# Kernel optimization log

Measured on AMD Instinct MI355X. Metric: run time of the kernel, lower is better.

The kernel has to match this reference:

```python
import jax, jax.numpy as jnp
import numpy as np

HEADS = 16
DIM_HEAD = 64
QUERY_DIM = 1024
INNER = HEADS * DIM_HEAD
SCALE = DIM_HEAD ** -0.5


def setup_inputs() -> dict:
    key = jax.random.key(0)
    ks = jax.random.split(key, 6)
    B, N, M = 2, 2048, 2048
    x = jax.random.normal(ks[0], (B, N, QUERY_DIM), dtype=jnp.float32)
    context = jax.random.normal(ks[1], (B, M, QUERY_DIM), dtype=jnp.float32)
    s = QUERY_DIM ** -0.5
    # weights stored [in, out] so y = x @ W matches torch Linear(x) with W = weight.T
    Wq = jax.random.normal(ks[2], (QUERY_DIM, INNER), dtype=jnp.float32) * s
    Wk = jax.random.normal(ks[3], (QUERY_DIM, INNER), dtype=jnp.float32) * s
    Wv = jax.random.normal(ks[4], (QUERY_DIM, INNER), dtype=jnp.float32) * s
    Wo = jax.random.normal(ks[5], (INNER, QUERY_DIM), dtype=jnp.float32) * (INNER ** -0.5)
    return {"x": x, "context": context, "Wq": Wq, "Wk": Wk, "Wv": Wv, "Wo": Wo}


def reference(x, context, Wq, Wk, Wv, Wo):
    B, N, _ = x.shape
    M = context.shape[1]
    # projections -> [b, n, h, d]
    q = (x @ Wq).reshape(B, N, HEADS, DIM_HEAD)
    k = (context @ Wk).reshape(B, M, HEADS, DIM_HEAD)
    v = (context @ Wv).reshape(B, M, HEADS, DIM_HEAD)
    sim = jnp.einsum('bihd,bjhd->bhij', q, k) * SCALE  # [b, h, n, m]
    attn = jax.nn.softmax(sim, axis=-1)
    out = jnp.einsum('bhij,bjhd->bihd', attn, v)  # [b, n, h, d]
    out = out.reshape(B, N, INNER)
    return out @ Wo
```

## Files before the change

kernel.cpp:

```cpp
#include <hip/hip_runtime.h>
#include <hip/hip_bf16.h>


typedef __attribute__((ext_vector_type(8))) __bf16    bf16x8;
typedef __attribute__((ext_vector_type(4))) __bf16    bf16x4;
typedef __attribute__((ext_vector_type(4))) float     f32x4;

#define B_    2
#define H_    16
#define N_    2048
#define M_    2048
#define D_    64
#define QD_   1024

#define QSCALE 0.18033688011112042f

__device__ __forceinline__ void gld16(const __bf16* g, __bf16* l) {
    __builtin_amdgcn_global_load_lds(
        (const __attribute__((address_space(1))) unsigned int*)(g),
        (__attribute__((address_space(3))) unsigned int*)(l), 16, 0, 0);
}

__global__ __launch_bounds__(256) void prep(const float* __restrict__ x,
                                            const float* __restrict__ ctx,
                                            const float* __restrict__ w0,
                                            const float* __restrict__ w1,
                                            const float* __restrict__ w2,
                                            const float* __restrict__ w3,
                                            __bf16* __restrict__ xb,
                                            __bf16* __restrict__ cb,
                                            __bf16* __restrict__ t0,
                                            __bf16* __restrict__ t1,
                                            __bf16* __restrict__ t2,
                                            __bf16* __restrict__ t3) {
    __shared__ float tile[64][65];
    const int z = blockIdx.z;
    if (z < 2) {
        const float* src = z ? ctx : x;
        __bf16*      dst = z ? cb  : xb;
        const size_t base = (size_t)(blockIdx.y * 16 + blockIdx.x) * 16384;
#pragma unroll
        for (int p = 0; p < 16; ++p) {
            size_t i = base + p * 1024 + threadIdx.x * 4;
            float4 v = *reinterpret_cast<const float4*>(src + i);
            bf16x4 o;
            o.x = (__bf16)v.x; o.y = (__bf16)v.y; o.z = (__bf16)v.z; o.w = (__bf16)v.w;
            *reinterpret_cast<bf16x4*>(dst + i) = o;
        }
        return;
    }
    const int w = z - 2;
    const float* in = (w == 0) ? w0 : (w == 1) ? w1 : (w == 2) ? w2 : w3;
    __bf16*     out = (w == 0) ? t0 : (w == 1) ? t1 : (w == 2) ? t2 : t3;
    const int i0 = blockIdx.x * 64;
    const int o0 = blockIdx.y * 64;
    const int t  = threadIdx.x;
    const int r  = t >> 4;
    const int c4 = (t & 15) * 4;
#pragma unroll
    for (int p = 0; p < 4; ++p) {
        int row = p * 16 + r;
        float4 v = *reinterpret_cast<const float4*>(in + (size_t)(i0 + row) * QD_ + o0 + c4);
        tile[row][c4 + 0] = v.x; tile[row][c4 + 1] = v.y;
        tile[row][c4 + 2] = v.z; tile[row][c4 + 3] = v.w;
    }
    __syncthreads();
#pragma unroll
    for (int p = 0; p < 4; ++p) {
        int orow = p * 16 + r;
        bf16x4 o;
        o.x = (__bf16)tile[c4 + 0][orow];
        o.y = (__bf16)tile[c4 + 1][orow];
        o.z = (__bf16)tile[c4 + 2][orow];
        o.w = (__bf16)tile[c4 + 3][orow];
        *reinterpret_cast<bf16x4*>(out + (size_t)(o0 + orow) * QD_ + i0 + c4) = o;
    }
}

#define GEMM_BODY(A_, Bt_)                                                                     \
    __shared__ __align__(16) __bf16 Alds[2][128 * 32];                                         \
    __shared__ __align__(16) __bf16 Blds[2][64 * 32];                                          \
    const int tid  = threadIdx.x;                                                              \
    const int wid  = tid >> 6;                                                                 \
    const int lane = tid & 63;                                                                 \
    const int l15  = lane & 15;                                                                \
    const int lg   = lane >> 4;                                                                \
    const int wr   = wid >> 1;                                                                 \
    const int wc   = wid & 1;                                                                  \
    const int rowBase = blockIdx.x * 128;                                                      \
    const int colBase = blockIdx.y * 64;                                                       \
    const int srowA = wid * 32 + (lane >> 2);                                                  \
    const int srowB = wid * 16 + (lane >> 2);                                                  \
    const int sgA   = ((lane & 3) ^ ((srowA >> 1) & 3)) * 8;                                   \
    const int sgB   = ((lane & 3) ^ ((srowB >> 1) & 3)) * 8;                                   \
    const __bf16* Ag  = A_  + (size_t)(rowBase + srowA) * QD_ + sgA;                           \
    const __bf16* Ag2 = Ag  + (size_t)16 * QD_;        \
    const __bf16* Bg  = Bt_ + (size_t)(colBase + srowB) * QD_ + sgB;                           \
    const int sOffA  = (wid * 32) * 32;                                                        \
    const int sOffA2 = sOffA + 16 * 32;                                                        \
    const int sOffB  = (wid * 16) * 32;                                                        \
    int aoff[4], boff[2];                                                                      \
    _Pragma("unroll")                                                                          \
    for (int m = 0; m < 4; ++m) {                                                              \
        int ra = wr * 64 + m * 16 + l15;                                                       \
        aoff[m] = ra * 32 + ((lg ^ ((ra >> 1) & 3)) * 8);                                      \
    }                                                                                          \
    _Pragma("unroll")                                                                          \
    for (int n = 0; n < 2; ++n) {                                                              \
        int rb = wc * 32 + n * 16 + l15;                                                       \
        boff[n] = rb * 32 + ((lg ^ ((rb >> 1) & 3)) * 8);                                      \
    }                                                                                          \
    f32x4 acc[4][2] = {};                                                                      \
    gld16(Ag,  &Alds[0][sOffA]);                                                               \
    gld16(Ag2, &Alds[0][sOffA2]);                                                              \
    gld16(Bg,  &Blds[0][sOffB]);                                                               \
    __syncthreads();                                                                           \
    for (int t = 0; t < 32; t += 2) {                                                          \
        if (t + 1 < 32) {                                                                      \
            int kn = (t + 1) * 32;                                                             \
            gld16(Ag + kn,  &Alds[1][sOffA]);                                                  \
            gld16(Ag2 + kn, &Alds[1][sOffA2]);                                                 \
            gld16(Bg + kn,  &Blds[1][sOffB]);                                                  \
        }                                                                                      \
        GCOMPUTE(0)                                                                            \
        __syncthreads();                                                                       \
        if (t + 2 < 32) {                                                                      \
            int kn = (t + 2) * 32;                                                             \
            gld16(Ag + kn,  &Alds[0][sOffA]);                                                  \
            gld16(Ag2 + kn, &Alds[0][sOffA2]);                                                 \
            gld16(Bg + kn,  &Blds[0][sOffB]);                                                  \
        }                                                                                      \
        GCOMPUTE(1)                                                                            \
        __syncthreads();                                                                       \
    }

#define GCOMPUTE(BUF)                                                                          \
    {                                                                                          \
        bf16x8 a[4], b[2];                                                                     \
        _Pragma("unroll")                                                                      \
        for (int m = 0; m < 4; ++m)                                                            \
            a[m] = *reinterpret_cast<const bf16x8*>(&Alds[BUF][aoff[m]]);                      \
        _Pragma("unroll")                                                                      \
        for (int n = 0; n < 2; ++n)                                                            \
            b[n] = *reinterpret_cast<const bf16x8*>(&Blds[BUF][boff[n]]);                      \
        _Pragma("unroll")                                                                      \
        for (int m = 0; m < 4; ++m)                                                            \
            _Pragma("unroll")                                                                  \
            for (int n = 0; n < 2; ++n)                                                        \
                acc[m][n] = __builtin_amdgcn_mfma_f32_16x16x32_bf16(a[m], b[n], acc[m][n], 0, 0, 0); \
    }

__global__ __launch_bounds__(256) void gemm_qkv(const __bf16* __restrict__ xb,
                                                const __bf16* __restrict__ cb,
                                                const __bf16* __restrict__ Wtq,
                                                const __bf16* __restrict__ Wtk,
                                                const __bf16* __restrict__ Wtv,
                                                __bf16* __restrict__ Qb,
                                                __bf16* __restrict__ Kb,
                                                __bf16* __restrict__ Vt) {
    const int z = blockIdx.z;
    const __bf16* Asel = (z == 0) ? xb : cb;
    const __bf16* Bsel = (z == 0) ? Wtq : (z == 1) ? Wtk : Wtv;
    GEMM_BODY(Asel, Bsel)
#pragma unroll
    for (int m = 0; m < 4; ++m)
#pragma unroll
        for (int n = 0; n < 2; ++n)
#pragma unroll
            for (int r = 0; r < 4; ++r) {
                int rr = rowBase + wr * 64 + m * 16 + lg * 4 + r;
                int cc = colBase + wc * 32 + n * 16 + l15;
                float v = acc[m][n][r];
                int b_ = rr >> 11, nn = rr & 2047, hh = cc >> 6, dd = cc & 63;
                if (z == 0) {
                    Qb[((size_t)(b_ * H_ + hh) * N_ + nn) * D_ + dd] = (__bf16)(v * QSCALE);
                } else if (z == 1) {
                    Kb[((size_t)(b_ * H_ + hh) * N_ + nn) * D_ + dd] = (__bf16)v;
                } else {
                    Vt[((size_t)(b_ * H_ + hh) * D_ + dd) * M_ + nn] = (__bf16)v;
                }
            }
}

__global__ __launch_bounds__(256) void gemm_out(const __bf16* __restrict__ AO,
                                                const __bf16* __restrict__ Wto,
                                                float* __restrict__ out) {
    GEMM_BODY(AO, Wto)
#pragma unroll
    for (int m = 0; m < 4; ++m)
#pragma unroll
        for (int n = 0; n < 2; ++n)
#pragma unroll
            for (int r = 0; r < 4; ++r) {
                int rr = rowBase + wr * 64 + m * 16 + lg * 4 + r;
                int cc = colBase + wc * 32 + n * 16 + l15;
                out[(size_t)rr * QD_ + cc] = acc[m][n][r];
            }
}

__global__ __launch_bounds__(512, 4) void attn_kernel(const __bf16* __restrict__ Q,
                                                      const __bf16* __restrict__ K,
                                                      const __bf16* __restrict__ Vt,
                                                      __bf16* __restrict__ AO) {
    __shared__ __align__(16) __bf16 Klds[2][4096];
    __shared__ __align__(16) __bf16 Vlds[2][4096];

    const int logical = (blockIdx.x & 7) * 64 + (blockIdx.x >> 3);
    const int qt   = logical & 15;
    const int bh   = logical >> 4;
    const int b    = bh >> 4;
    const int h    = bh & 15;
    const int wid  = threadIdx.x >> 6;
    const int lane = threadIdx.x & 63;
    const int l15  = lane & 15;
    const int lg   = lane >> 4;
    const int qbase = qt * 128 + wid * 16;

    const __bf16* Qp = Q  + ((size_t)bh * N_ + qbase) * D_;
    const __bf16* Kp = K  + (size_t)bh * M_ * D_;
    const __bf16* Vp = Vt + (size_t)bh * D_ * M_;

    const int rg   = lane >> 3;
    const int ch   = lane & 7;
    const int skw  = (rg & 3) | ((wid & 1) << 2);
    const int kc   = (ch ^ skw) << 3;
    const int vc   = (ch ^ rg) << 3;
    const int srow = wid * 8 + rg;
    const int ldst = wid * 512;

#define STAGE(BUF, KV0)                                                        \
    gld16(Kp + (size_t)((KV0) + srow) * D_ + kc, &Klds[BUF][ldst]);            \
    gld16(Vp + (size_t)srow * M_ + (KV0) + vc,  &Vlds[BUF][ldst]);

    const int rm0 = ((l15 >> 2) * 8) + (l15 & 3);
    const int sq  = (l15 & 7) << 3;
    const int ak00 = rm0 * 64 + (( 0 + lg * 8) ^ sq);
    const int ak01 = rm0 * 64 + ((32 + lg * 8) ^ sq);
    const int ak10 = ak00 + 256;
    const int ak11 = ak01 + 256;
    const int av0 = l15 * 64 + (( 0 + lg * 8) ^ sq);
    const int av1 = l15 * 64 + ((32 + lg * 8) ^ sq);

    bf16x8 qf0 = *reinterpret_cast<const bf16x8*>(Qp + (size_t)l15 * D_ +      lg * 8);
    bf16x8 qf1 = *reinterpret_cast<const bf16x8*>(Qp + (size_t)l15 * D_ + 32 + lg * 8);

    bf16x8 onesf;
#pragma unroll
    for (int j = 0; j < 8; ++j) onesf[j] = (__bf16)1.0f;

    f32x4 o0 = {}, o1 = {}, o2 = {}, o3 = {}, ors = {};

#define COMPUTE(KB, VB, KOFF, AV)                                                               \
    {                                                                                           \
        bf16x8 k00 = *reinterpret_cast<const bf16x8*>((KB) + ak00 + (KOFF));                    \
        bf16x8 k01 = *reinterpret_cast<const bf16x8*>((KB) + ak01 + (KOFF));                    \
        bf16x8 k10 = *reinterpret_cast<const bf16x8*>((KB) + ak10 + (KOFF));                    \
        bf16x8 k11 = *reinterpret_cast<const bf16x8*>((KB) + ak11 + (KOFF));                    \
        bf16x8 v0  = *reinterpret_cast<const bf16x8*>((VB) + (AV));                             \
        bf16x8 v1  = *reinterpret_cast<const bf16x8*>((VB) + (AV) + 1024);                      \
        bf16x8 v2  = *reinterpret_cast<const bf16x8*>((VB) + (AV) + 2048);                      \
        bf16x8 v3  = *reinterpret_cast<const bf16x8*>((VB) + (AV) + 3072);                      \
        f32x4 s0 = {}, s1 = {};                                                                 \
        s0 = __builtin_amdgcn_mfma_f32_16x16x32_bf16(k00, qf0, s0, 0, 0, 0);                    \
        s0 = __builtin_amdgcn_mfma_f32_16x16x32_bf16(k01, qf1, s0, 0, 0, 0);                    \
        s1 = __builtin_amdgcn_mfma_f32_16x16x32_bf16(k10, qf0, s1, 0, 0, 0);                    \
        s1 = __builtin_amdgcn_mfma_f32_16x16x32_bf16(k11, qf1, s1, 0, 0, 0);                    \
        bf16x8 pf;                                                                              \
        pf[0] = (__bf16)__builtin_amdgcn_exp2f(s0[0]);                                          \
        pf[1] = (__bf16)__builtin_amdgcn_exp2f(s0[1]);                                          \
        pf[2] = (__bf16)__builtin_amdgcn_exp2f(s0[2]);                                          \
        pf[3] = (__bf16)__builtin_amdgcn_exp2f(s0[3]);                                          \
        pf[4] = (__bf16)__builtin_amdgcn_exp2f(s1[0]);                                          \
        pf[5] = (__bf16)__builtin_amdgcn_exp2f(s1[1]);                                          \
        pf[6] = (__bf16)__builtin_amdgcn_exp2f(s1[2]);                                          \
        pf[7] = (__bf16)__builtin_amdgcn_exp2f(s1[3]);                                          \
        ors = __builtin_amdgcn_mfma_f32_16x16x32_bf16(pf, onesf, ors, 0, 0, 0);                 \
        o0 = __builtin_amdgcn_mfma_f32_16x16x32_bf16(pf, v0, o0, 0, 0, 0);                      \
        o1 = __builtin_amdgcn_mfma_f32_16x16x32_bf16(pf, v1, o1, 0, 0, 0);                      \
        o2 = __builtin_amdgcn_mfma_f32_16x16x32_bf16(pf, v2, o2, 0, 0, 0);                      \
        o3 = __builtin_amdgcn_mfma_f32_16x16x32_bf16(pf, v3, o3, 0, 0, 0);                      \
    }

    STAGE(0, 0)
    __syncthreads();

    for (int t = 0; t < 32; t += 2) {
        if (t + 1 < 32) { STAGE(1, (t + 1) * 64) }
        COMPUTE(Klds[0], Vlds[0], 0,    av0)
        COMPUTE(Klds[0], Vlds[0], 2048, av1)
        __syncthreads();
        if (t + 2 < 32) { STAGE(0, (t + 2) * 64) }
        COMPUTE(Klds[1], Vlds[1], 0,    av0)
        COMPUTE(Klds[1], Vlds[1], 2048, av1)
        __syncthreads();
    }
#undef STAGE
#undef COMPUTE

#pragma unroll
    for (int r = 0; r < 4; ++r) {
        float inv = 1.0f / ors[r];
        size_t row = ((size_t)b * N_ + qbase + lg * 4 + r) * QD_ + h * D_ + l15;
        AO[row +  0] = (__bf16)(o0[r] * inv);
        AO[row + 16] = (__bf16)(o1[r] * inv);
        AO[row + 32] = (__bf16)(o2[r] * inv);
        AO[row + 48] = (__bf16)(o3[r] * inv);
    }
}

extern "C" void kernel_launch(void* const* d_in, const int* in_sizes, int n_in,
                              void* d_out, int out_size, void* d_ws, size_t ws_size,
                              hipStream_t stream) {
    const float* x   = (const float*)d_in[0];
    const float* ctx = (const float*)d_in[1];
    const float* Wq  = (const float*)d_in[2];
    const float* Wk  = (const float*)d_in[3];
    const float* Wv  = (const float*)d_in[4];
    const float* Wo  = (const float*)d_in[5];

    char* ws = (char*)d_ws;
    __bf16* xb  = (__bf16*)(ws);
    __bf16* cb  = (__bf16*)(ws + (8u  << 20));
    __bf16* Wtq = (__bf16*)(ws + (16u << 20));
    __bf16* Wtk = (__bf16*)(ws + (18u << 20));
    __bf16* Wtv = (__bf16*)(ws + (20u << 20));
    __bf16* Wto = (__bf16*)(ws + (22u << 20));
    __bf16* Qb  = (__bf16*)(ws + (24u << 20));
    __bf16* Kb  = (__bf16*)(ws + (32u << 20));
    __bf16* Vt  = (__bf16*)(ws + (40u << 20));
    __bf16* AO  = (__bf16*)(ws + (48u << 20));

    prep<<<dim3(16, 16, 6), 256, 0, stream>>>(x, ctx, Wq, Wk, Wv, Wo,
                                              xb, cb, Wtq, Wtk, Wtv, Wto);
    gemm_qkv<<<dim3(32, 16, 3), 256, 0, stream>>>(xb, cb, Wtq, Wtk, Wtv, Qb, Kb, Vt);
    attn_kernel<<<512, 512, 0, stream>>>(Qb, Kb, Vt, AO);
    gemm_out<<<dim3(32, 16), 256, 0, stream>>>(AO, Wto, (float*)d_out);
}
```

Measured before the change: 124.6 us.

## Enlarge QKV GEMM tile and stage GEMM epilogues through LDS

The QKV projection GEMM tile grows from 128x64 to 128x128, giving each wave a 4x4 MFMA accumulator grid and halving the grid in y, which doubles reuse of each A tile. Both GEMM epilogues now stage accumulators in shared memory and write out with 16-byte vector stores, replacing scattered 2-byte and 4-byte stores. This matters most for the transposed V layout, where the old per-element stores were strided by M. The cost is more accumulator registers, a larger LDS pool and an extra barrier per block.

New measurement: 109.1 us. 12.4% less time.

```diff
diff --git a/kernel.cpp b/kernel.cpp
--- a/kernel.cpp
+++ b/kernel.cpp
@@ -77,79 +77,6 @@
     }
 }
 
-#define GEMM_BODY(A_, Bt_)                                                                     \
-    __shared__ __align__(16) __bf16 Alds[2][128 * 32];                                         \
-    __shared__ __align__(16) __bf16 Blds[2][64 * 32];                                          \
-    const int tid  = threadIdx.x;                                                              \
-    const int wid  = tid >> 6;                                                                 \
-    const int lane = tid & 63;                                                                 \
-    const int l15  = lane & 15;                                                                \
-    const int lg   = lane >> 4;                                                                \
-    const int wr   = wid >> 1;                                                                 \
-    const int wc   = wid & 1;                                                                  \
-    const int rowBase = blockIdx.x * 128;                                                      \
-    const int colBase = blockIdx.y * 64;                                                       \
-    const int srowA = wid * 32 + (lane >> 2);                                                  \
-    const int srowB = wid * 16 + (lane >> 2);                                                  \
-    const int sgA   = ((lane & 3) ^ ((srowA >> 1) & 3)) * 8;                                   \
-    const int sgB   = ((lane & 3) ^ ((srowB >> 1) & 3)) * 8;                                   \
-    const __bf16* Ag  = A_  + (size_t)(rowBase + srowA) * QD_ + sgA;                           \
-    const __bf16* Ag2 = Ag  + (size_t)16 * QD_;        \
-    const __bf16* Bg  = Bt_ + (size_t)(colBase + srowB) * QD_ + sgB;                           \
-    const int sOffA  = (wid * 32) * 32;                                                        \
-    const int sOffA2 = sOffA + 16 * 32;                                                        \
-    const int sOffB  = (wid * 16) * 32;                                                        \
-    int aoff[4], boff[2];                                                                      \
-    _Pragma("unroll")                                                                          \
-    for (int m = 0; m < 4; ++m) {                                                              \
-        int ra = wr * 64 + m * 16 + l15;                                                       \
-        aoff[m] = ra * 32 + ((lg ^ ((ra >> 1) & 3)) * 8);                                      \
-    }                                                                                          \
-    _Pragma("unroll")                                                                          \
-    for (int n = 0; n < 2; ++n) {                                                              \
-        int rb = wc * 32 + n * 16 + l15;                                                       \
-        boff[n] = rb * 32 + ((lg ^ ((rb >> 1) & 3)) * 8);                                      \
-    }                                                                                          \
-    f32x4 acc[4][2] = {};                                                                      \
-    gld16(Ag,  &Alds[0][sOffA]);                                                               \
-    gld16(Ag2, &Alds[0][sOffA2]);                                                              \
-    gld16(Bg,  &Blds[0][sOffB]);                                                               \
-    __syncthreads();                                                                           \
-    for (int t = 0; t < 32; t += 2) {                                                          \
-        if (t + 1 < 32) {                                                                      \
-            int kn = (t + 1) * 32;                                                             \
-            gld16(Ag + kn,  &Alds[1][sOffA]);                                                  \
-            gld16(Ag2 + kn, &Alds[1][sOffA2]);                                                 \
-            gld16(Bg + kn,  &Blds[1][sOffB]);                                                  \
-        }                                                                                      \
-        GCOMPUTE(0)                                                                            \
-        __syncthreads();                                                                       \
-        if (t + 2 < 32) {                                                                      \
-            int kn = (t + 2) * 32;                                                             \
-            gld16(Ag + kn,  &Alds[0][sOffA]);                                                  \
-            gld16(Ag2 + kn, &Alds[0][sOffA2]);                                                 \
-            gld16(Bg + kn,  &Blds[0][sOffB]);                                                  \
-        }                                                                                      \
-        GCOMPUTE(1)                                                                            \
-        __syncthreads();                                                                       \
-    }
-
-#define GCOMPUTE(BUF)                                                                          \
-    {                                                                                          \
-        bf16x8 a[4], b[2];                                                                     \
-        _Pragma("unroll")                                                                      \
-        for (int m = 0; m < 4; ++m)                                                            \
-            a[m] = *reinterpret_cast<const bf16x8*>(&Alds[BUF][aoff[m]]);                      \
-        _Pragma("unroll")                                                                      \
-        for (int n = 0; n < 2; ++n)                                                            \
-            b[n] = *reinterpret_cast<const bf16x8*>(&Blds[BUF][boff[n]]);                      \
-        _Pragma("unroll")                                                                      \
-        for (int m = 0; m < 4; ++m)                                                            \
-            _Pragma("unroll")                                                                  \
-            for (int n = 0; n < 2; ++n)                                                        \
-                acc[m][n] = __builtin_amdgcn_mfma_f32_16x16x32_bf16(a[m], b[n], acc[m][n], 0, 0, 0); \
-    }
-
 __global__ __launch_bounds__(256) void gemm_qkv(const __bf16* __restrict__ xb,
                                                 const __bf16* __restrict__ cb,
                                                 const __bf16* __restrict__ Wtq,
@@ -158,44 +85,221 @@
                                                 __bf16* __restrict__ Qb,
                                                 __bf16* __restrict__ Kb,
                                                 __bf16* __restrict__ Vt) {
+    __shared__ __align__(16) __bf16 POOL[16384];
+    __bf16* const Al0 = POOL;
+    __bf16* const Al1 = POOL + 4096;
+    __bf16* const Bl0 = POOL + 8192;
+    __bf16* const Bl1 = POOL + 12288;
+
     const int z = blockIdx.z;
-    const __bf16* Asel = (z == 0) ? xb : cb;
-    const __bf16* Bsel = (z == 0) ? Wtq : (z == 1) ? Wtk : Wtv;
-    GEMM_BODY(Asel, Bsel)
+    const __bf16* A_  = (z == 0) ? xb : cb;
+    const __bf16* Bt_ = (z == 0) ? Wtq : (z == 1) ? Wtk : Wtv;
+
+    const int tid  = threadIdx.x;
+    const int wid  = tid >> 6;
+    const int lane = tid & 63;
+    const int l15  = lane & 15;
+    const int lg   = lane >> 4;
+    const int wr   = wid >> 1;
+    const int wc   = wid & 1;
+    const int rowBase = blockIdx.x * 128;
+    const int colBase = blockIdx.y * 128;
+    const int srow = wid * 32 + (lane >> 2);
+    const int sg   = ((lane & 3) ^ ((srow >> 1) & 3)) * 8;
+    const __bf16* Ag  = A_  + (size_t)(rowBase + srow) * QD_ + sg;
+    const __bf16* Ag2 = Ag  + (size_t)16 * QD_;
+    const __bf16* Bg  = Bt_ + (size_t)(colBase + srow) * QD_ + sg;
+    const __bf16* Bg2 = Bg  + (size_t)16 * QD_;
+    const int sOff  = (wid * 32) * 32;
+    const int sOff2 = sOff + 16 * 32;
+    int aoff[4], boff[4];
+#pragma unroll
+    for (int m = 0; m < 4; ++m) {
+        int ra = wr * 64 + m * 16 + l15;
+        int rb = wc * 64 + m * 16 + l15;
+        aoff[m] = ra * 32 + ((lg ^ ((ra >> 1) & 3)) * 8);
+        boff[m] = rb * 32 + ((lg ^ ((rb >> 1) & 3)) * 8);
+    }
+    f32x4 acc[4][4] = {};
+
+#define GCOMPUTE(AL, BL)                                                                       \
+    {                                                                                          \
+        bf16x8 a[4], b[4];                                                                     \
+        _Pragma("unroll")                                                                      \
+        for (int m = 0; m < 4; ++m)                                                            \
+            a[m] = *reinterpret_cast<const bf16x8*>(&(AL)[aoff[m]]);                           \
+        _Pragma("unroll")                                                                      \
+        for (int n = 0; n < 4; ++n)                                                            \
+            b[n] = *reinterpret_cast<const bf16x8*>(&(BL)[boff[n]]);                           \
+        _Pragma("unroll")                                                                      \
+        for (int m = 0; m < 4; ++m)                                                            \
+            _Pragma("unroll")                                                                  \
+            for (int n = 0; n < 4; ++n)                                                        \
+                acc[m][n] = __builtin_amdgcn_mfma_f32_16x16x32_bf16(a[m], b[n], acc[m][n], 0, 0, 0); \
+    }
+
+    gld16(Ag,  Al0 + sOff);
+    gld16(Ag2, Al0 + sOff2);
+    gld16(Bg,  Bl0 + sOff);
+    gld16(Bg2, Bl0 + sOff2);
+    __syncthreads();
+    for (int t = 0; t < 32; t += 2) {
+        if (t + 1 < 32) {
+            int kn = (t + 1) * 32;
+            gld16(Ag + kn,  Al1 + sOff);
+            gld16(Ag2 + kn, Al1 + sOff2);
+            gld16(Bg + kn,  Bl1 + sOff);
+            gld16(Bg2 + kn, Bl1 + sOff2);
+        }
+        GCOMPUTE(Al0, Bl0)
+        __syncthreads();
+        if (t + 2 < 32) {
+            int kn = (t + 2) * 32;
+            gld16(Ag + kn,  Al0 + sOff);
+            gld16(Ag2 + kn, Al0 + sOff2);
+            gld16(Bg + kn,  Bl0 + sOff);
+            gld16(Bg2 + kn, Bl0 + sOff2);
+        }
+        GCOMPUTE(Al1, Bl1)
+        __syncthreads();
+    }
+#undef GCOMPUTE
+
 #pragma unroll
     for (int m = 0; m < 4; ++m)
 #pragma unroll
-        for (int n = 0; n < 2; ++n)
+        for (int n = 0; n < 4; ++n)
 #pragma unroll
             for (int r = 0; r < 4; ++r) {
-                int rr = rowBase + wr * 64 + m * 16 + lg * 4 + r;
-                int cc = colBase + wc * 32 + n * 16 + l15;
                 float v = acc[m][n][r];
-                int b_ = rr >> 11, nn = rr & 2047, hh = cc >> 6, dd = cc & 63;
-                if (z == 0) {
-                    Qb[((size_t)(b_ * H_ + hh) * N_ + nn) * D_ + dd] = (__bf16)(v * QSCALE);
-                } else if (z == 1) {
-                    Kb[((size_t)(b_ * H_ + hh) * N_ + nn) * D_ + dd] = (__bf16)v;
-                } else {
-                    Vt[((size_t)(b_ * H_ + hh) * D_ + dd) * M_ + nn] = (__bf16)v;
-                }
+                if (z == 0) v *= QSCALE;
+                int rl = wr * 64 + m * 16 + lg * 4 + r;
+                int cl = wc * 64 + n * 16 + l15;
+                if (z == 2) POOL[cl * 128 + rl] = (__bf16)v;
+                else        POOL[rl * 128 + cl] = (__bf16)v;
             }
+    __syncthreads();
+
+    const int prow0 = tid >> 4;
+    const int pcol  = (tid & 15) * 8;
+#pragma unroll
+    for (int s = 0; s < 8; ++s) {
+        int row = s * 16 + prow0;
+        bf16x8 vv = *reinterpret_cast<const bf16x8*>(&POOL[row * 128 + pcol]);
+        if (z == 2) {
+            int cc = colBase + row, rr = rowBase + pcol;
+            int b_ = rr >> 11, mm = rr & 2047, hh = cc >> 6, dd = cc & 63;
+            *reinterpret_cast<bf16x8*>(&Vt[((size_t)(b_ * H_ + hh) * D_ + dd) * M_ + mm]) = vv;
+        } else {
+            int rr = rowBase + row, cc = colBase + pcol;
+            int b_ = rr >> 11, nn = rr & 2047, hh = cc >> 6, dd = cc & 63;
+            __bf16* dst = (z == 0) ? Qb : Kb;
+            *reinterpret_cast<bf16x8*>(&dst[((size_t)(b_ * H_ + hh) * N_ + nn) * D_ + dd]) = vv;
+        }
+    }
 }
 
 __global__ __launch_bounds__(256) void gemm_out(const __bf16* __restrict__ AO,
                                                 const __bf16* __restrict__ Wto,
                                                 float* __restrict__ out) {
-    GEMM_BODY(AO, Wto)
+    __shared__ __align__(16) __bf16 POOL[16384];
+    __bf16* const Al0 = POOL;
+    __bf16* const Al1 = POOL + 4096;
+    __bf16* const Bl0 = POOL + 8192;
+    __bf16* const Bl1 = POOL + 10240;
+
+    const int tid  = threadIdx.x;
+    const int wid  = tid >> 6;
+    const int lane = tid & 63;
+    const int l15  = lane & 15;
+    const int lg   = lane >> 4;
+    const int wr   = wid >> 1;
+    const int wc   = wid & 1;
+    const int rowBase = blockIdx.x * 128;
+    const int colBase = blockIdx.y * 64;
+    const int srowA = wid * 32 + (lane >> 2);
+    const int srowB = wid * 16 + (lane >> 2);
+    const int sgA   = ((lane & 3) ^ ((srowA >> 1) & 3)) * 8;
+    const int sgB   = ((lane & 3) ^ ((srowB >> 1) & 3)) * 8;
+    const __bf16* Ag  = AO  + (size_t)(rowBase + srowA) * QD_ + sgA;
+    const __bf16* Ag2 = Ag  + (size_t)16 * QD_;
+    const __bf16* Bg  = Wto + (size_t)(colBase + srowB) * QD_ + sgB;
+    const int sOffA  = (wid * 32) * 32;
+    const int sOffA2 = sOffA + 16 * 32;
+    const int sOffB  = (wid * 16) * 32;
+    int aoff[4], boff[2];
+#pragma unroll
+    for (int m = 0; m < 4; ++m) {
+        int ra = wr * 64 + m * 16 + l15;
+        aoff[m] = ra * 32 + ((lg ^ ((ra >> 1) & 3)) * 8);
+    }
+#pragma unroll
+    for (int n = 0; n < 2; ++n) {
+        int rb = wc * 32 + n * 16 + l15;
+        boff[n] = rb * 32 + ((lg ^ ((rb >> 1) & 3)) * 8);
+    }
+    f32x4 acc[4][2] = {};
+
+#define GCOMPUTE2(AL, BL)                                                                      \
+    {                                                                                          \
+        bf16x8 a[4], b[2];                                                                     \
+        _Pragma("unroll")                                                                      \
+        for (int m = 0; m < 4; ++m)                                                            \
+            a[m] = *reinterpret_cast<const bf16x8*>(&(AL)[aoff[m]]);                           \
+        _Pragma("unroll")                                                                      \
+        for (int n = 0; n < 2; ++n)                                                            \
+            b[n] = *reinterpret_cast<const bf16x8*>(&(BL)[boff[n]]);                           \
+        _Pragma("unroll")                                                                      \
+        for (int m = 0; m < 4; ++m)                                                            \
+            _Pragma("unroll")                                                                  \
+            for (int n = 0; n < 2; ++n)                                                        \
+                acc[m][n] = __builtin_amdgcn_mfma_f32_16x16x32_bf16(a[m], b[n], acc[m][n], 0, 0, 0); \
+    }
+
+    gld16(Ag,  Al0 + sOffA);
+    gld16(Ag2, Al0 + sOffA2);
+    gld16(Bg,  Bl0 + sOffB);
+    __syncthreads();
+    for (int t = 0; t < 32; t += 2) {
+        if (t + 1 < 32) {
+            int kn = (t + 1) * 32;
+            gld16(Ag + kn,  Al1 + sOffA);
+            gld16(Ag2 + kn, Al1 + sOffA2);
+            gld16(Bg + kn,  Bl1 + sOffB);
+        }
+        GCOMPUTE2(Al0, Bl0)
+        __syncthreads();
+        if (t + 2 < 32) {
+            int kn = (t + 2) * 32;
+            gld16(Ag + kn,  Al0 + sOffA);
+            gld16(Ag2 + kn, Al0 + sOffA2);
+            gld16(Bg + kn,  Bl0 + sOffB);
+        }
+        GCOMPUTE2(Al1, Bl1)
+        __syncthreads();
+    }
+#undef GCOMPUTE2
+
+    float* FP = reinterpret_cast<float*>(POOL);
 #pragma unroll
     for (int m = 0; m < 4; ++m)
 #pragma unroll
         for (int n = 0; n < 2; ++n)
 #pragma unroll
             for (int r = 0; r < 4; ++r) {
-                int rr = rowBase + wr * 64 + m * 16 + lg * 4 + r;
-                int cc = colBase + wc * 32 + n * 16 + l15;
-                out[(size_t)rr * QD_ + cc] = acc[m][n][r];
+                int rl = wr * 64 + m * 16 + lg * 4 + r;
+                int cl = wc * 32 + n * 16 + l15;
+                FP[rl * 64 + cl] = acc[m][n][r];
             }
+    __syncthreads();
+    const int prow0 = tid >> 4;
+    const int pcol4 = (tid & 15) * 4;
+#pragma unroll
+    for (int s = 0; s < 8; ++s) {
+        int row = s * 16 + prow0;
+        float4 vv = *reinterpret_cast<const float4*>(&FP[row * 64 + pcol4]);
+        *reinterpret_cast<float4*>(&out[(size_t)(rowBase + row) * QD_ + colBase + pcol4]) = vv;
+    }
 }
 
 __global__ __launch_bounds__(512, 4) void attn_kernel(const __bf16* __restrict__ Q,
@@ -332,7 +436,7 @@
 
     prep<<<dim3(16, 16, 6), 256, 0, stream>>>(x, ctx, Wq, Wk, Wv, Wo,
                                               xb, cb, Wtq, Wtk, Wtv, Wto);
-    gemm_qkv<<<dim3(32, 16, 3), 256, 0, stream>>>(xb, cb, Wtq, Wtk, Wtv, Qb, Kb, Vt);
+    gemm_qkv<<<dim3(32, 8, 3), 256, 0, stream>>>(xb, cb, Wtq, Wtk, Wtv, Qb, Kb, Vt);
     attn_kernel<<<512, 512, 0, stream>>>(Qb, Kb, Vt, AO);
     gemm_out<<<dim3(32, 16), 256, 0, stream>>>(AO, Wto, (float*)d_out);
 }
```
